# Kernel tuning notes

Hardware: AMD Instinct MI355X
Metric: run time of the kernel (lower is better)

The kernel has to match this reference:

```python
import jax, jax.numpy as jnp
import numpy as np

# Static ragged shape parameters (seq_len is a static list in the original op)
SEQ_LEN = (1024, 2048, 512, 1536)
HEAD_NUM = 16


def setup_inputs() -> dict:
    key = jax.random.key(0)
    total = HEAD_NUM * sum(s * s for s in SEQ_LEN)  # 125,829,120 elems
    x = jax.random.normal(key, (total,), dtype=jnp.float32)
    return {"x": x, "seq_len": SEQ_LEN, "head_num": HEAD_NUM}


def reference(x, seq_len, head_num):
    """Packed variable-length softmax.

    x is the flat concatenation over batches b of blocks of shape
    (head_num, s_b, s_b); softmax is taken over the last (row) dimension
    of each block. seq_len/head_num are static Python values, so the
    per-segment offsets and slice shapes are static (jit-compatible).
    """
    outs = []
    off = 0
    for s in seq_len:  # loop over small static batch list, not data dims
        n = head_num * s * s
        # rows of length s; softmax over each row (numerically stable)
        blk = x[off:off + n].reshape(head_num * s, s)
        outs.append(jax.nn.softmax(blk, axis=-1).reshape(-1))
        off += n
    return jnp.concatenate(outs)
```

## Files before the change

kernel.cpp:

```cpp
#include <hip/hip_runtime.h>
#include <math.h>


#define NROWS 81920

__global__ __launch_bounds__(256) void fast_softmax_kernel(
    const float* __restrict__ x, float* __restrict__ out) {
    const int row = blockIdx.x;

    int s, r, base;
    if (row < 16384)      { s = 1024; base = 0;        r = row;         }
    else if (row < 49152) { s = 2048; base = 16777216; r = row - 16384; }
    else if (row < 57344) { s = 512;  base = 83886080; r = row - 49152; }
    else                  { s = 1536; base = 88080384; r = row - 57344; }

    const int elem0 = base + r * s;
    const float4* __restrict__ rowp = (const float4*)(x + elem0);
    float4* __restrict__ outp = (float4*)(out + elem0);
    const int nv4 = s >> 2;
    const int tid = threadIdx.x;

    float4 v[2];
    float lmax = -INFINITY;
    int cnt = 0;
    #pragma unroll 2
    for (int i = tid; i < nv4; i += 256) {
        float4 t = rowp[i];
        v[cnt++] = t;
        lmax = fmaxf(lmax, fmaxf(fmaxf(t.x, t.y), fmaxf(t.z, t.w)));
    }

    __shared__ float smax[4];
    __shared__ float ssum[4];
    #pragma unroll
    for (int off = 32; off > 0; off >>= 1)
        lmax = fmaxf(lmax, __shfl_xor(lmax, off, 64));
    const int wid  = tid >> 6;
    const int lane = tid & 63;
    if (lane == 0) smax[wid] = lmax;
    __syncthreads();
    const float m = fmaxf(fmaxf(smax[0], smax[1]), fmaxf(smax[2], smax[3]));

    float lsum = 0.0f;
    #pragma unroll
    for (int k = 0; k < cnt; ++k) {
        float4 t = v[k];
        t.x = __expf(t.x - m);
        t.y = __expf(t.y - m);
        t.z = __expf(t.z - m);
        t.w = __expf(t.w - m);
        v[k] = t;
        lsum += (t.x + t.y) + (t.z + t.w);
    }

    #pragma unroll
    for (int off = 32; off > 0; off >>= 1)
        lsum += __shfl_xor(lsum, off, 64);
    if (lane == 0) ssum[wid] = lsum;
    __syncthreads();
    const float total = (ssum[0] + ssum[1]) + (ssum[2] + ssum[3]);
    const float inv = 1.0f / total;

    cnt = 0;
    #pragma unroll 2
    for (int i = tid; i < nv4; i += 256) {
        float4 t = v[cnt++];
        t.x *= inv; t.y *= inv; t.z *= inv; t.w *= inv;
        outp[i] = t;
    }
}

extern "C" void kernel_launch(void* const* d_in, const int* in_sizes, int n_in,
                              void* d_out, int out_size, void* d_ws, size_t ws_size,
                              hipStream_t stream) {
    const float* x = (const float*)d_in[0];
    float* out = (float*)d_out;
    fast_softmax_kernel<<<NROWS, 256, 0, stream>>>(x, out);
}
```

Measured before the change: 772.5 us.

## Map one wavefront per softmax row with templated row length and nontemporal stores

The work mapping changes from one 256-thread block per row to one 64-lane wavefront per row, four rows per block. Reductions become pure wave shuffles, so the shared memory and __syncthreads barriers go away. Row length is a template parameter, so the per-lane loads are fully unrolled into registers, up to 8 float4 per lane for 2048-wide rows. Output uses nontemporal stores to reduce cache pollution on this streaming kernel. The trade-offs are more registers per thread and load imbalance between waves in the same block when the rows differ in length.

```diff
diff --git a/kernel.cpp b/kernel.cpp
--- a/kernel.cpp
+++ b/kernel.cpp
@@ -2,71 +2,74 @@
 #include <math.h>
 
 
+typedef float f32x4 __attribute__((ext_vector_type(4)));
+
 #define NROWS 81920
+#define NBLOCKS (NROWS / 4)
 
-__global__ __launch_bounds__(256) void fast_softmax_kernel(
-    const float* __restrict__ x, float* __restrict__ out) {
-    const int row = blockIdx.x;
+template <int S>
+__device__ __forceinline__ void softmax_row_wave(
+    const float* __restrict__ rowf, float* __restrict__ outf, int lane) {
+    constexpr int PER = S / 4 / 64;
+    const f32x4* __restrict__ rowp = (const f32x4*)rowf;
+    f32x4* __restrict__ outp = (f32x4*)outf;
 
-    int s, r, base;
-    if (row < 16384)      { s = 1024; base = 0;        r = row;         }
-    else if (row < 49152) { s = 2048; base = 16777216; r = row - 16384; }
-    else if (row < 57344) { s = 512;  base = 83886080; r = row - 49152; }
-    else                  { s = 1536; base = 88080384; r = row - 57344; }
-
-    const int elem0 = base + r * s;
-    const float4* __restrict__ rowp = (const float4*)(x + elem0);
-    float4* __restrict__ outp = (float4*)(out + elem0);
-    const int nv4 = s >> 2;
-    const int tid = threadIdx.x;
-
-    float4 v[2];
+    f32x4 v[PER];
     float lmax = -INFINITY;
-    int cnt = 0;
-    #pragma unroll 2
-    for (int i = tid; i < nv4; i += 256) {
-        float4 t = rowp[i];
-        v[cnt++] = t;
+#pragma unroll
+    for (int k = 0; k < PER; ++k) {
+        f32x4 t = rowp[lane + 64 * k];
+        v[k] = t;
         lmax = fmaxf(lmax, fmaxf(fmaxf(t.x, t.y), fmaxf(t.z, t.w)));
     }
 
-    __shared__ float smax[4];
-    __shared__ float ssum[4];
-    #pragma unroll
-    for (int off = 32; off > 0; off >>= 1)
+#pragma unroll
+    for (int off = 32; off; off >>= 1)
         lmax = fmaxf(lmax, __shfl_xor(lmax, off, 64));
-    const int wid  = tid >> 6;
-    const int lane = tid & 63;
-    if (lane == 0) smax[wid] = lmax;
-    __syncthreads();
-    const float m = fmaxf(fmaxf(smax[0], smax[1]), fmaxf(smax[2], smax[3]));
 
     float lsum = 0.0f;
-    #pragma unroll
-    for (int k = 0; k < cnt; ++k) {
-        float4 t = v[k];
-        t.x = __expf(t.x - m);
-        t.y = __expf(t.y - m);
-        t.z = __expf(t.z - m);
-        t.w = __expf(t.w - m);
+#pragma unroll
+    for (int k = 0; k < PER; ++k) {
+        f32x4 t = v[k];
+        t.x = __expf(t.x - lmax);
+        t.y = __expf(t.y - lmax);
+        t.z = __expf(t.z - lmax);
+        t.w = __expf(t.w - lmax);
         v[k] = t;
         lsum += (t.x + t.y) + (t.z + t.w);
     }
 
-    #pragma unroll
-    for (int off = 32; off > 0; off >>= 1)
+#pragma unroll
+    for (int off = 32; off; off >>= 1)
         lsum += __shfl_xor(lsum, off, 64);
-    if (lane == 0) ssum[wid] = lsum;
-    __syncthreads();
-    const float total = (ssum[0] + ssum[1]) + (ssum[2] + ssum[3]);
-    const float inv = 1.0f / total;
+    const float inv = 1.0f / lsum;
 
-    cnt = 0;
-    #pragma unroll 2
-    for (int i = tid; i < nv4; i += 256) {
-        float4 t = v[cnt++];
+#pragma unroll
+    for (int k = 0; k < PER; ++k) {
+        f32x4 t = v[k];
         t.x *= inv; t.y *= inv; t.z *= inv; t.w *= inv;
-        outp[i] = t;
+        __builtin_nontemporal_store(t, &outp[lane + 64 * k]);
+    }
+}
+
+__global__ __launch_bounds__(256) void fast_softmax_kernel(
+    const float* __restrict__ x, float* __restrict__ out) {
+    const int wid  = threadIdx.x >> 6;
+    const int lane = threadIdx.x & 63;
+    const int row  = (blockIdx.x << 2) + wid;
+
+    if (row < 16384) {
+        const int e0 = row << 10;
+        softmax_row_wave<1024>(x + e0, out + e0, lane);
+    } else if (row < 49152) {
+        const int e0 = 16777216 + ((row - 16384) << 11);
+        softmax_row_wave<2048>(x + e0, out + e0, lane);
+    } else if (row < 57344) {
+        const int e0 = 83886080 + ((row - 49152) << 9);
+        softmax_row_wave<512>(x + e0, out + e0, lane);
+    } else {
+        const int e0 = 88080384 + (row - 57344) * 1536;
+        softmax_row_wave<1536>(x + e0, out + e0, lane);
     }
 }
 
@@ -75,5 +78,5 @@
                               hipStream_t stream) {
     const float* x = (const float*)d_in[0];
     float* out = (float*)d_out;
-    fast_softmax_kernel<<<NROWS, 256, 0, stream>>>(x, out);
+    fast_softmax_kernel<<<NBLOCKS, 256, 0, stream>>>(x, out);
 }
```

After: 805.3 us. 4.2% more time.
